# Optimization experiments

Measured on AMD Instinct MI355X. Metric: run time of the kernel, lower is better.

## Reference

```python
import jax, jax.numpy as jnp
import numpy as np

T, N, C, D, S = 512, 32, 1296, 512, 30
NORM_SCALE = 32.0
NEGINF = -1e9


def setup_inputs() -> dict:
    key = jax.random.key(0)
    k1, k2, k3, k4, k5 = jax.random.split(key, 5)
    feats = jax.random.normal(k1, (T * N, D), dtype=jnp.float32)
    classifier_weight = jax.random.normal(k2, (D, C), dtype=jnp.float32)
    labeling = jax.random.randint(k3, (N, S), 1, C)  # targets cannot be blank(0)
    logit_lgts = (T - jax.random.randint(k4, (N,), 0, 32)).astype(jnp.int32)
    labeling_lgts = (S - jax.random.randint(k5, (N,), 0, 5)).astype(jnp.int32)
    return dict(feats=feats, classifier_weight=classifier_weight,
                labeling=labeling, logit_lgts=logit_lgts, labeling_lgts=labeling_lgts)


def _ctc_loss(log_probs, labels, in_lens, lab_lens):
    # log_probs: (T, N, C); labels: (N, S); blank = 0; reduction = 'sum'
    Tt, Nn, Cc = log_probs.shape
    Ss = labels.shape[1]
    L = 2 * Ss + 1
    # extended labeling: blank, l1, blank, l2, ..., blank  -> (N, L)
    ext = jnp.zeros((Nn, L), dtype=labels.dtype).at[:, 1::2].set(labels)
    # gather per-state log-probs: (T, N, L)
    lp_ext = jnp.take_along_axis(log_probs, jnp.broadcast_to(ext[None], (Tt, Nn, L)), axis=2)
    # skip transition s-2 -> s allowed iff s > 1 and ext[s] != ext[s-2]
    skip_ok = jnp.concatenate(
        [jnp.zeros((Nn, 2), dtype=bool), ext[:, 2:] != ext[:, :-2]], axis=1)
    alpha0 = (jnp.full((Nn, L), NEGINF, dtype=log_probs.dtype)
              .at[:, 0].set(lp_ext[0, :, 0])
              .at[:, 1].set(lp_ext[0, :, 1]))

    def step(alpha, inp):
        lp_t, t = inp  # lp_t: (N, L)
        a1 = alpha
        a2 = jnp.pad(alpha[:, :-1], ((0, 0), (1, 0)), constant_values=NEGINF)
        a3 = jnp.where(skip_ok,
                       jnp.pad(alpha[:, :-2], ((0, 0), (2, 0)), constant_values=NEGINF),
                       NEGINF)
        new = jax.nn.logsumexp(jnp.stack([a1, a2, a3], axis=0), axis=0) + lp_t
        # freeze alpha once t reaches a sample's input length
        alpha = jnp.where((t < in_lens)[:, None], new, alpha)
        return alpha, None

    alpha, _ = jax.lax.scan(step, alpha0, (lp_ext[1:], jnp.arange(1, Tt)))
    Ln = 2 * lab_lens + 1  # (N,)
    last = jnp.take_along_axis(alpha, (Ln - 1)[:, None], axis=1)[:, 0]
    last2 = jnp.take_along_axis(alpha, (Ln - 2)[:, None], axis=1)[:, 0]
    nll = -jnp.logaddexp(last, last2)
    return jnp.sum(nll)


def reference(feats, classifier_weight, labeling, logit_lgts, labeling_lgts):
    # RadialCTC: cosine logits with norm_scale, then CTC on log-softmax.
    w_n = classifier_weight / jnp.linalg.norm(classifier_weight, axis=0, keepdims=True)  # (D, C)
    f_n = feats / jnp.linalg.norm(feats, axis=1, keepdims=True)  # (T*N, D)
    logits = NORM_SCALE * (f_n @ w_n)  # (T*N, C)
    log_probs = jax.nn.log_softmax(logits.reshape(T, N, C), axis=-1)
    return _ctc_loss(log_probs, labeling, logit_lgts, labeling_lgts)
```

## Files before the change

kernel.cpp:

```cpp
#include <hip/hip_runtime.h>
#include <stdint.h>
#include <stddef.h>


typedef _Float16 f16;
typedef _Float16 f16x8 __attribute__((ext_vector_type(8)));
typedef float f32x4 __attribute__((ext_vector_type(4)));
typedef __attribute__((address_space(1))) void* as1_void_ptr;
typedef __attribute__((address_space(3))) void* as3_void_ptr;

#define TT 512
#define NN 32
#define CC 1296
#define DD 512
#define SS 30
#define CP 1408
#define LL 61
#define NORM_SCALE 32.0f
#define LOG2E 1.4426950408889634f
#define LN2   0.6931471805599453f

#define PREP_WBLK (CP / 16)
#define PREP_ZBLK 17
#define PREP_FBLK (TT * NN / 4)

#define GEMM_BLK ((TT * NN / 128) * (CP / 128))
#define GATH_BLK (NN * (TT / 64))

__device__ __forceinline__ float fexp2(float x) { return __builtin_amdgcn_exp2f(x); }
__device__ __forceinline__ float flog2(float x) { return __builtin_amdgcn_logf(x); }

__device__ __forceinline__ double dpp_sr1_zero64(double x) {
    long long b = __double_as_longlong(x);
    int lo = (int)(b & 0xFFFFFFFFLL);
    int hi = (int)(b >> 32);
    int lo2 = __builtin_amdgcn_update_dpp(0, lo, 0x138, 0xF, 0xF, false);
    int hi2 = __builtin_amdgcn_update_dpp(0, hi, 0x138, 0xF, 0xF, false);
    return __longlong_as_double(((long long)hi2 << 32) |
                                (unsigned long long)(unsigned int)lo2);
}
template <int CTRL>
__device__ __forceinline__ int dpp_imax_level(int m) {
    int t = __builtin_amdgcn_update_dpp(0, m, CTRL, 0xF, 0xF, false);
    return m > t ? m : t;
}

__global__ __launch_bounds__(256) void prep_kernel(const float* __restrict__ W,
                                                   const float* __restrict__ feats,
                                                   f16* __restrict__ wt,
                                                   f16* __restrict__ fn,
                                                   float* __restrict__ sumexp,
                                                   unsigned* __restrict__ ctr) {
    int bx = blockIdx.x, tid = threadIdx.x;
    if (bx < PREP_WBLK) {
        __shared__ float red[256];
        __shared__ float rqs[16];
        int c0 = bx * 16;
        int cl = tid & 15, dg = tid >> 4;
        int c = c0 + cl;
        float ss = 0.f;
        if (c < CC) {
            for (int d = dg; d < DD; d += 16) {
                float v = W[(size_t)d * CC + c];
                ss += v * v;
            }
        }
        red[tid] = ss;
        __syncthreads();
        if (tid < 16) {
            float s2 = 0.f;
            #pragma unroll
            for (int k = 0; k < 16; ++k) s2 += red[tid + 16 * k];
            rqs[tid] = rsqrtf(s2);
        }
        __syncthreads();
        int c_loc = tid >> 4, dl = tid & 15;
        int cc = c0 + c_loc;
        float rq = rqs[c_loc];
        #pragma unroll 4
        for (int it = 0; it < 32; ++it) {
            int d = dl + it * 16;
            float v = (cc < CC) ? W[(size_t)d * CC + cc] * rq : 0.f;
            wt[(size_t)cc * DD + d] = (f16)v;
        }
    } else if (bx < PREP_WBLK + PREP_ZBLK) {
        int zb = bx - PREP_WBLK;
        if (zb < 16) {
            float4 z = {0.f, 0.f, 0.f, 0.f};
            ((float4*)sumexp)[zb * 256 + tid] = z;
        } else if (tid == 0) {
            *ctr = 0u;
        }
    } else {
        int fb = bx - PREP_WBLK - PREP_ZBLK;
        int wv = (fb * 256 + tid) >> 6;
        int lane = tid & 63;
        const float4* src = (const float4*)(feats + (size_t)wv * DD) + lane * 2;
        float4 a = src[0], b = src[1];
        float ss = a.x*a.x + a.y*a.y + a.z*a.z + a.w*a.w
                 + b.x*b.x + b.y*b.y + b.z*b.z + b.w*b.w;
        #pragma unroll
        for (int off = 32; off; off >>= 1) ss += __shfl_xor(ss, off);
        float r = rsqrtf(ss);
        f16x8 o;
        o[0]=(f16)(a.x*r); o[1]=(f16)(a.y*r); o[2]=(f16)(a.z*r); o[3]=(f16)(a.w*r);
        o[4]=(f16)(b.x*r); o[5]=(f16)(b.y*r); o[6]=(f16)(b.z*r); o[7]=(f16)(b.w*r);
        *(f16x8*)(fn + (size_t)wv * DD + lane * 8) = o;
    }
}

__global__ __launch_bounds__(256) void gg_kernel(const f16* __restrict__ A,
                                                 const f16* __restrict__ B,
                                                 const int* __restrict__ labels,
                                                 float* __restrict__ sumexp,
                                                 float* __restrict__ lp_lab) {
    __shared__ __align__(16) f16 sm[8192];
    int bx = blockIdx.x;
    int tid = threadIdx.x;
    int w = tid >> 6, lane = tid & 63;
    int lm = lane & 15, hi = lane >> 4;
    int sw = (lm >> 1) & 3;

    if (bx < GEMM_BLK) {
        int bm = bx & 127, bn = bx >> 7;
        int wm = w >> 1, wn = w & 1;
        f32x4 acc[4][4];
        f32x4 zero = {0.f, 0.f, 0.f, 0.f};
        #pragma unroll
        for (int i = 0; i < 4; ++i)
            #pragma unroll
            for (int j = 0; j < 4; ++j) acc[i][j] = zero;

        for (int kb = 0; kb < 16; ++kb) {
            #pragma unroll
            for (int p = 0; p < 2; ++p) {
                int s = p * 256 + tid;
                int row = s >> 2;
                int ch = (s & 3) ^ ((row >> 1) & 3);
                const f16* ga = A + (size_t)(bm * 128 + row) * DD + kb * 32 + ch * 8;
                const f16* gb = B + (size_t)(bn * 128 + row) * DD + kb * 32 + ch * 8;
                __builtin_amdgcn_global_load_lds((as1_void_ptr)ga,
                    (as3_void_ptr)&sm[(p * 256 + w * 64) * 8], 16, 0, 0);
                __builtin_amdgcn_global_load_lds((as1_void_ptr)gb,
                    (as3_void_ptr)&sm[4096 + (p * 256 + w * 64) * 8], 16, 0, 0);
            }
            __syncthreads();
            f16x8 af[4], bf[4];
            #pragma unroll
            for (int i = 0; i < 4; ++i)
                af[i] = *(const f16x8*)&sm[(wm * 64 + i * 16 + lm) * 32 + (hi ^ sw) * 8];
            #pragma unroll
            for (int j = 0; j < 4; ++j)
                bf[j] = *(const f16x8*)&sm[4096 + (wn * 64 + j * 16 + lm) * 32 + (hi ^ sw) * 8];
            #pragma unroll
            for (int i = 0; i < 4; ++i)
                #pragma unroll
                for (int j = 0; j < 4; ++j)
                    acc[i][j] = __builtin_amdgcn_mfma_f32_16x16x32_f16(af[i], bf[j], acc[i][j], 0, 0, 0);
            __syncthreads();
        }
        #pragma unroll
        for (int i = 0; i < 4; ++i) {
            float rs[4] = {0.f, 0.f, 0.f, 0.f};
            #pragma unroll
            for (int j = 0; j < 4; ++j) {
                int c = bn * 128 + wn * 64 + j * 16 + lm;
                bool ok = (c < CC);
                #pragma unroll
                for (int r = 0; r < 4; ++r)
                    rs[r] += ok ? fexp2(acc[i][j][r] * (NORM_SCALE * LOG2E)) : 0.f;
            }
            #pragma unroll
            for (int off = 1; off < 16; off <<= 1) {
                #pragma unroll
                for (int r = 0; r < 4; ++r) rs[r] += __shfl_xor(rs[r], off);
            }
            if (lm == 0) {
                int rowb = bm * 128 + wm * 64 + i * 16 + hi * 4;
                #pragma unroll
                for (int r = 0; r < 4; ++r) atomicAdd(&sumexp[rowb + r], rs[r]);
            }
        }
    } else {
        int gbx = bx - GEMM_BLK;
        int n = gbx & 31, t0 = (gbx >> 5) * 64;
        int arow = tid >> 2;
        int ach = (tid & 3) ^ ((arow >> 1) & 3);
        const f16* gaB = A + (size_t)((t0 + arow) * NN + n) * DD + ach * 8;
        int brow = tid >> 2;
        int bch = (tid & 3) ^ ((brow >> 1) & 3);
        int cls = (brow == 0 || brow > SS) ? 0 : labels[n * SS + brow - 1];
        const f16* gbB = B + (size_t)cls * DD + bch * 8;

        f32x4 acc0 = {0.f, 0.f, 0.f, 0.f};
        f32x4 acc1 = {0.f, 0.f, 0.f, 0.f};
        for (int kb = 0; kb < 16; ++kb) {
            __builtin_amdgcn_global_load_lds((as1_void_ptr)(gaB + kb * 32),
                (as3_void_ptr)&sm[tid * 8], 16, 0, 0);
            if (tid < 128)
                __builtin_amdgcn_global_load_lds((as1_void_ptr)(gbB + kb * 32),
                    (as3_void_ptr)&sm[2048 + tid * 8], 16, 0, 0);
            __syncthreads();
            f16x8 af  = *(const f16x8*)&sm[(w * 16 + lm) * 32 + (hi ^ sw) * 8];
            f16x8 bf0 = *(const f16x8*)&sm[2048 + lm * 32 + (hi ^ sw) * 8];
            f16x8 bf1 = *(const f16x8*)&sm[2048 + (16 + lm) * 32 + (hi ^ sw) * 8];
            acc0 = __builtin_amdgcn_mfma_f32_16x16x32_f16(af, bf0, acc0, 0, 0, 0);
            acc1 = __builtin_amdgcn_mfma_f32_16x16x32_f16(af, bf1, acc1, 0, 0, 0);
            __syncthreads();
        }
        #pragma unroll
        for (int jn = 0; jn < 2; ++jn) {
            int j = jn * 16 + lm;
            if (j >= 31) continue;
            float* dst = lp_lab + ((size_t)n * 31 + j) * TT + t0;
            f32x4 av = jn ? acc1 : acc0;
            #pragma unroll
            for (int r = 0; r < 4; ++r) {
                int tl = w * 16 + hi * 4 + r;
                dst[tl] = av[r] * (NORM_SCALE * LOG2E);
            }
        }
    }
}

__global__ void ctc_kernel(const float* __restrict__ lp_lab, const int* __restrict__ labels,
                           const int* __restrict__ in_lens, const int* __restrict__ lab_lens,
                           const float* __restrict__ sumexp,
                           float* __restrict__ nll, unsigned* __restrict__ ctr,
                           float* __restrict__ out) {
    int n = blockIdx.x;
    int s = threadIdx.x;
    bool valid = s < LL;
    int ext = (valid && (s & 1)) ? labels[n * SS + (s >> 1)] : 0;
    int jmap = (valid && (s & 1)) ? ((s >> 1) + 1) : 0;
    int ext2 = __shfl_up(ext, 2);
    double skipd = ((s >= 2) && valid && (ext != ext2)) ? 1.0 : 0.0;
    int Tin = in_lens[n];
    const float4* g0 = (const float4*)(lp_lab + ((size_t)n * 31 + jmap) * TT);

    float4 cur = g0[0];
    float4 nxt = g0[1];
    float4 nx2 = g0[2];
    double beta = (s <= 1) ? (double)fexp2(cur.x) : 0.0;
    int Mi = 0;

    auto stepL = [&](float lp) {
        double P = (double)fexp2(lp);
        double b1 = dpp_sr1_zero64(beta);
        double b2 = dpp_sr1_zero64(b1);
        beta = (beta + b1 + b2 * skipd) * P;
    };
    auto renorm = [&]() {
        int h = (int)(__double_as_longlong(beta) >> 32);
        h = dpp_imax_level<0x111>(h);
        h = dpp_imax_level<0x112>(h);
        h = dpp_imax_level<0x114>(h);
        h = dpp_imax_level<0x118>(h);
        int r0 = __builtin_amdgcn_readlane(h, 15);
        int r1 = __builtin_amdgcn_readlane(h, 31);
        int r2 = __builtin_amdgcn_readlane(h, 47);
        int r3 = __builtin_amdgcn_readlane(h, 63);
        int mx = max(max(r0, r1), max(r2, r3));
        int e11 = mx >> 20;
        double scale = __longlong_as_double((long long)(2046 - e11) << 52);
        beta *= scale;
        Mi += e11 - 1023;
    };

    stepL(cur.y); stepL(cur.z); stepL(cur.w);
    renorm();
    int remaining = Tin - 4;
    int g = 1;
    while (remaining >= 4) {
        cur = nxt; nxt = nx2;
        int gi = g + 2; if (gi > 127) gi = 127;
        nx2 = g0[gi];
        stepL(cur.x); stepL(cur.y); stepL(cur.z); stepL(cur.w);
        renorm();
        remaining -= 4; ++g;
    }
    cur = nxt;
    if (remaining > 0) stepL(cur.x);
    if (remaining > 1) stepL(cur.y);
    if (remaining > 2) stepL(cur.z);

    double ms = 0.0;
    for (int t = s; t < Tin; t += 64)
        ms += (double)flog2(sumexp[(size_t)t * NN + n]);
    #pragma unroll
    for (int off = 32; off; off >>= 1) ms += __shfl_xor(ms, off);

    int Ln = 2 * lab_lens[n] + 1;
    double last  = __shfl(beta, Ln - 1);
    double last2 = __shfl(beta, Ln - 2);
    double sm = last + last2;
    long long bb = __double_as_longlong(sm);
    int e = (int)(bb >> 52) - 1023;
    double mant = __longlong_as_double((bb & 0xFFFFFFFFFFFFFLL) | (1023LL << 52));
    float v = (float)(-((double)flog2((float)mant) + (double)(e + Mi) - ms) * LN2);
    if (s == 0) {
        nll[n] = v;
        __threadfence();
        unsigned old = atomicAdd(ctr, 1u);
        if (old == NN - 1) {
            __threadfence();
            float t = 0.f;
            for (int i = 0; i < NN; ++i) t += nll[i];
            out[0] = t;
        }
    }
}

extern "C" void kernel_launch(void* const* d_in, const int* in_sizes, int n_in,
                              void* d_out, int out_size, void* d_ws, size_t ws_size,
                              hipStream_t stream) {
    const float* feats        = (const float*)d_in[0];
    const float* W            = (const float*)d_in[1];
    const int*   labeling     = (const int*)d_in[2];
    const int*   logit_lgts   = (const int*)d_in[3];
    const int*   labeling_lgts= (const int*)d_in[4];
    float* out = (float*)d_out;
    char* ws = (char*)d_ws;

    size_t off = 0;
    f16*   wt     = (f16*)(ws + off);   off += (size_t)CP * DD * 2;
    f16*   fn     = (f16*)(ws + off);   off += (size_t)TT * NN * DD * 2;
    float* sumexp = (float*)(ws + off); off += (size_t)TT * NN * 4;
    float* lp_lab = (float*)(ws + off); off += (size_t)NN * 31 * TT * 4;
    float* nllb   = (float*)(ws + off); off += 64 * 4;
    unsigned* ctr = (unsigned*)(ws + off); off += 64;

    prep_kernel<<<PREP_WBLK + PREP_ZBLK + PREP_FBLK, 256, 0, stream>>>(
        W, feats, wt, fn, sumexp, ctr);
    gg_kernel<<<GEMM_BLK + GATH_BLK, 256, 0, stream>>>(fn, wt, labeling, sumexp, lp_lab);
    ctc_kernel<<<NN, 64, 0, stream>>>(lp_lab, labeling, logit_lgts, labeling_lgts,
                                      sumexp, nllb, ctr, out);

    (void)in_sizes; (void)n_in; (void)out_size; (void)ws_size;
}
```

Baseline: 160.7 us.

## Fuse CTC recursion into GEMM kernel with atomic-counter cross-block signaling

Merges the GEMM/gather kernel and the CTC kernel into one launch. The 32 CTC blocks come first in the grid and spin on a counter until the gather blocks finish, then run the alpha recursion while the GEMM blocks are still computing the softmax sums, and wait on a second counter only before the final normalisation. This overlaps the serial CTC recursion with the GEMM and removes one launch. The cost is that 32 blocks occupy CU slots while spinning, and correctness depends on those blocks being scheduled alongside the producer blocks.

New measurement: 312.2 us. 1.94x slower.

```diff
diff --git a/kernel.cpp b/kernel.cpp
--- a/kernel.cpp
+++ b/kernel.cpp
@@ -26,9 +26,21 @@
 
 #define GEMM_BLK ((TT * NN / 128) * (CP / 128))
 #define GATH_BLK (NN * (TT / 64))
+#define MEGA_CTC 32
+#define MEGA_GATH0 MEGA_CTC
+#define MEGA_GEMM0 (MEGA_CTC + GATH_BLK)
+#define MEGA_BLK  (MEGA_GEMM0 + GEMM_BLK)
 
 __device__ __forceinline__ float fexp2(float x) { return __builtin_amdgcn_exp2f(x); }
 __device__ __forceinline__ float flog2(float x) { return __builtin_amdgcn_logf(x); }
+
+__device__ __forceinline__ void wait_cnt(unsigned* p, unsigned target) {
+    while (__hip_atomic_load(p, __ATOMIC_ACQUIRE, __HIP_MEMORY_SCOPE_AGENT) < target)
+        __builtin_amdgcn_s_sleep(8);
+}
+__device__ __forceinline__ void post_cnt(unsigned* p) {
+    __hip_atomic_fetch_add(p, 1u, __ATOMIC_RELEASE, __HIP_MEMORY_SCOPE_AGENT);
+}
 
 __device__ __forceinline__ double dpp_sr1_zero64(double x) {
     long long b = __double_as_longlong(x);
@@ -50,7 +62,7 @@
                                                    f16* __restrict__ wt,
                                                    f16* __restrict__ fn,
                                                    float* __restrict__ sumexp,
-                                                   unsigned* __restrict__ ctr) {
+                                                   unsigned* __restrict__ cnt) {
     int bx = blockIdx.x, tid = threadIdx.x;
     if (bx < PREP_WBLK) {
         __shared__ float red[256];
@@ -88,8 +100,8 @@
         if (zb < 16) {
             float4 z = {0.f, 0.f, 0.f, 0.f};
             ((float4*)sumexp)[zb * 256 + tid] = z;
-        } else if (tid == 0) {
-            *ctr = 0u;
+        } else if (tid < 3) {
+            cnt[tid] = 0u;
         }
     } else {
         int fb = bx - PREP_WBLK - PREP_ZBLK;
@@ -109,11 +121,16 @@
     }
 }
 
-__global__ __launch_bounds__(256) void gg_kernel(const f16* __restrict__ A,
-                                                 const f16* __restrict__ B,
-                                                 const int* __restrict__ labels,
-                                                 float* __restrict__ sumexp,
-                                                 float* __restrict__ lp_lab) {
+__global__ __launch_bounds__(256) void mega_kernel(const f16* __restrict__ A,
+                                                   const f16* __restrict__ B,
+                                                   const int* __restrict__ labels,
+                                                   const int* __restrict__ in_lens,
+                                                   const int* __restrict__ lab_lens,
+                                                   float* __restrict__ sumexp,
+                                                   float* __restrict__ lp_lab,
+                                                   float* __restrict__ nll,
+                                                   unsigned* __restrict__ cnt,
+                                                   float* __restrict__ out) {
     __shared__ __align__(16) f16 sm[8192];
     int bx = blockIdx.x;
     int tid = threadIdx.x;
@@ -121,15 +138,16 @@
     int lm = lane & 15, hi = lane >> 4;
     int sw = (lm >> 1) & 3;
 
-    if (bx < GEMM_BLK) {
-        int bm = bx & 127, bn = bx >> 7;
+    if (bx >= MEGA_GEMM0) {
+        int j = bx - MEGA_GEMM0;
+        int bm = j & 127, bn = j >> 7;
         int wm = w >> 1, wn = w & 1;
         f32x4 acc[4][4];
         f32x4 zero = {0.f, 0.f, 0.f, 0.f};
         #pragma unroll
         for (int i = 0; i < 4; ++i)
             #pragma unroll
-            for (int j = 0; j < 4; ++j) acc[i][j] = zero;
+            for (int jj = 0; jj < 4; ++jj) acc[i][jj] = zero;
 
         for (int kb = 0; kb < 16; ++kb) {
             #pragma unroll
@@ -150,25 +168,25 @@
             for (int i = 0; i < 4; ++i)
                 af[i] = *(const f16x8*)&sm[(wm * 64 + i * 16 + lm) * 32 + (hi ^ sw) * 8];
             #pragma unroll
-            for (int j = 0; j < 4; ++j)
-                bf[j] = *(const f16x8*)&sm[4096 + (wn * 64 + j * 16 + lm) * 32 + (hi ^ sw) * 8];
+            for (int jj = 0; jj < 4; ++jj)
+                bf[jj] = *(const f16x8*)&sm[4096 + (wn * 64 + jj * 16 + lm) * 32 + (hi ^ sw) * 8];
             #pragma unroll
             for (int i = 0; i < 4; ++i)
                 #pragma unroll
-                for (int j = 0; j < 4; ++j)
-                    acc[i][j] = __builtin_amdgcn_mfma_f32_16x16x32_f16(af[i], bf[j], acc[i][j], 0, 0, 0);
+                for (int jj = 0; jj < 4; ++jj)
+                    acc[i][jj] = __builtin_amdgcn_mfma_f32_16x16x32_f16(af[i], bf[jj], acc[i][jj], 0, 0, 0);
             __syncthreads();
         }
         #pragma unroll
         for (int i = 0; i < 4; ++i) {
             float rs[4] = {0.f, 0.f, 0.f, 0.f};
             #pragma unroll
-            for (int j = 0; j < 4; ++j) {
-                int c = bn * 128 + wn * 64 + j * 16 + lm;
+            for (int jj = 0; jj < 4; ++jj) {
+                int c = bn * 128 + wn * 64 + jj * 16 + lm;
                 bool ok = (c < CC);
                 #pragma unroll
                 for (int r = 0; r < 4; ++r)
-                    rs[r] += ok ? fexp2(acc[i][j][r] * (NORM_SCALE * LOG2E)) : 0.f;
+                    rs[r] += ok ? fexp2(acc[i][jj][r] * (NORM_SCALE * LOG2E)) : 0.f;
             }
             #pragma unroll
             for (int off = 1; off < 16; off <<= 1) {
@@ -181,8 +199,11 @@
                 for (int r = 0; r < 4; ++r) atomicAdd(&sumexp[rowb + r], rs[r]);
             }
         }
-    } else {
-        int gbx = bx - GEMM_BLK;
+        __threadfence();
+        __syncthreads();
+        if (tid == 0) post_cnt(&cnt[1]);
+    } else if (bx >= MEGA_GATH0) {
+        int gbx = bx - MEGA_GATH0;
         int n = gbx & 31, t0 = (gbx >> 5) * 64;
         int arow = tid >> 2;
         int ach = (tid & 3) ^ ((arow >> 1) & 3);
@@ -210,9 +231,9 @@
         }
         #pragma unroll
         for (int jn = 0; jn < 2; ++jn) {
-            int j = jn * 16 + lm;
-            if (j >= 31) continue;
-            float* dst = lp_lab + ((size_t)n * 31 + j) * TT + t0;
+            int jc = jn * 16 + lm;
+            if (jc >= 31) continue;
+            float* dst = lp_lab + ((size_t)n * 31 + jc) * TT + t0;
             f32x4 av = jn ? acc1 : acc0;
             #pragma unroll
             for (int r = 0; r < 4; ++r) {
@@ -220,93 +241,94 @@
                 dst[tl] = av[r] * (NORM_SCALE * LOG2E);
             }
         }
-    }
-}
-
-__global__ void ctc_kernel(const float* __restrict__ lp_lab, const int* __restrict__ labels,
-                           const int* __restrict__ in_lens, const int* __restrict__ lab_lens,
-                           const float* __restrict__ sumexp,
-                           float* __restrict__ nll, unsigned* __restrict__ ctr,
-                           float* __restrict__ out) {
-    int n = blockIdx.x;
-    int s = threadIdx.x;
-    bool valid = s < LL;
-    int ext = (valid && (s & 1)) ? labels[n * SS + (s >> 1)] : 0;
-    int jmap = (valid && (s & 1)) ? ((s >> 1) + 1) : 0;
-    int ext2 = __shfl_up(ext, 2);
-    double skipd = ((s >= 2) && valid && (ext != ext2)) ? 1.0 : 0.0;
-    int Tin = in_lens[n];
-    const float4* g0 = (const float4*)(lp_lab + ((size_t)n * 31 + jmap) * TT);
-
-    float4 cur = g0[0];
-    float4 nxt = g0[1];
-    float4 nx2 = g0[2];
-    double beta = (s <= 1) ? (double)fexp2(cur.x) : 0.0;
-    int Mi = 0;
-
-    auto stepL = [&](float lp) {
-        double P = (double)fexp2(lp);
-        double b1 = dpp_sr1_zero64(beta);
-        double b2 = dpp_sr1_zero64(b1);
-        beta = (beta + b1 + b2 * skipd) * P;
-    };
-    auto renorm = [&]() {
-        int h = (int)(__double_as_longlong(beta) >> 32);
-        h = dpp_imax_level<0x111>(h);
-        h = dpp_imax_level<0x112>(h);
-        h = dpp_imax_level<0x114>(h);
-        h = dpp_imax_level<0x118>(h);
-        int r0 = __builtin_amdgcn_readlane(h, 15);
-        int r1 = __builtin_amdgcn_readlane(h, 31);
-        int r2 = __builtin_amdgcn_readlane(h, 47);
-        int r3 = __builtin_amdgcn_readlane(h, 63);
-        int mx = max(max(r0, r1), max(r2, r3));
-        int e11 = mx >> 20;
-        double scale = __longlong_as_double((long long)(2046 - e11) << 52);
-        beta *= scale;
-        Mi += e11 - 1023;
-    };
-
-    stepL(cur.y); stepL(cur.z); stepL(cur.w);
-    renorm();
-    int remaining = Tin - 4;
-    int g = 1;
-    while (remaining >= 4) {
-        cur = nxt; nxt = nx2;
-        int gi = g + 2; if (gi > 127) gi = 127;
-        nx2 = g0[gi];
-        stepL(cur.x); stepL(cur.y); stepL(cur.z); stepL(cur.w);
+        __threadfence();
+        __syncthreads();
+        if (tid == 0) post_cnt(&cnt[0]);
+    } else if (tid < 64) {
+        int n = bx;
+        int s = tid;
+        wait_cnt(&cnt[0], GATH_BLK);
+
+        bool valid = s < LL;
+        int ext = (valid && (s & 1)) ? labels[n * SS + (s >> 1)] : 0;
+        int jmap = (valid && (s & 1)) ? ((s >> 1) + 1) : 0;
+        int ext2 = __shfl_up(ext, 2);
+        double skipd = ((s >= 2) && valid && (ext != ext2)) ? 1.0 : 0.0;
+        int Tin = in_lens[n];
+        const float4* g0 = (const float4*)(lp_lab + ((size_t)n * 31 + jmap) * TT);
+
+        float4 cur = g0[0];
+        float4 nxt = g0[1];
+        float4 nx2 = g0[2];
+        double beta = (s <= 1) ? (double)fexp2(cur.x) : 0.0;
+        int Mi = 0;
+
+        auto stepL = [&](float lp) {
+            double P = (double)fexp2(lp);
+            double b1 = dpp_sr1_zero64(beta);
+            double b2 = dpp_sr1_zero64(b1);
+            beta = (beta + b1 + b2 * skipd) * P;
+        };
+        auto renorm = [&]() {
+            int h = (int)(__double_as_longlong(beta) >> 32);
+            h = dpp_imax_level<0x111>(h);
+            h = dpp_imax_level<0x112>(h);
+            h = dpp_imax_level<0x114>(h);
+            h = dpp_imax_level<0x118>(h);
+            int r0 = __builtin_amdgcn_readlane(h, 15);
+            int r1 = __builtin_amdgcn_readlane(h, 31);
+            int r2 = __builtin_amdgcn_readlane(h, 47);
+            int r3 = __builtin_amdgcn_readlane(h, 63);
+            int mx = max(max(r0, r1), max(r2, r3));
+            int e11 = mx >> 20;
+            double scale = __longlong_as_double((long long)(2046 - e11) << 52);
+            beta *= scale;
+            Mi += e11 - 1023;
+        };
+
+        stepL(cur.y); stepL(cur.z); stepL(cur.w);
         renorm();
-        remaining -= 4; ++g;
-    }
-    cur = nxt;
-    if (remaining > 0) stepL(cur.x);
-    if (remaining > 1) stepL(cur.y);
-    if (remaining > 2) stepL(cur.z);
-
-    double ms = 0.0;
-    for (int t = s; t < Tin; t += 64)
-        ms += (double)flog2(sumexp[(size_t)t * NN + n]);
-    #pragma unroll
-    for (int off = 32; off; off >>= 1) ms += __shfl_xor(ms, off);
-
-    int Ln = 2 * lab_lens[n] + 1;
-    double last  = __shfl(beta, Ln - 1);
-    double last2 = __shfl(beta, Ln - 2);
-    double sm = last + last2;
-    long long bb = __double_as_longlong(sm);
-    int e = (int)(bb >> 52) - 1023;
-    double mant = __longlong_as_double((bb & 0xFFFFFFFFFFFFFLL) | (1023LL << 52));
-    float v = (float)(-((double)flog2((float)mant) + (double)(e + Mi) - ms) * LN2);
-    if (s == 0) {
-        nll[n] = v;
-        __threadfence();
-        unsigned old = atomicAdd(ctr, 1u);
-        if (old == NN - 1) {
+        int remaining = Tin - 4;
+        int g = 1;
+        while (remaining >= 4) {
+            cur = nxt; nxt = nx2;
+            int gi = g + 2; if (gi > 127) gi = 127;
+            nx2 = g0[gi];
+            stepL(cur.x); stepL(cur.y); stepL(cur.z); stepL(cur.w);
+            renorm();
+            remaining -= 4; ++g;
+        }
+        cur = nxt;
+        if (remaining > 0) stepL(cur.x);
+        if (remaining > 1) stepL(cur.y);
+        if (remaining > 2) stepL(cur.z);
+
+        wait_cnt(&cnt[1], GEMM_BLK);
+
+        double ms = 0.0;
+        for (int t = s; t < Tin; t += 64)
+            ms += (double)flog2(sumexp[(size_t)t * NN + n]);
+        #pragma unroll
+        for (int off = 32; off; off >>= 1) ms += __shfl_xor(ms, off);
+
+        int Ln = 2 * lab_lens[n] + 1;
+        double last  = __shfl(beta, Ln - 1);
+        double last2 = __shfl(beta, Ln - 2);
+        double smv = last + last2;
+        long long bb = __double_as_longlong(smv);
+        int e = (int)(bb >> 52) - 1023;
+        double mant = __longlong_as_double((bb & 0xFFFFFFFFFFFFFLL) | (1023LL << 52));
+        float v = (float)(-((double)flog2((float)mant) + (double)(e + Mi) - ms) * LN2);
+        if (s == 0) {
+            nll[n] = v;
             __threadfence();
-            float t = 0.f;
-            for (int i = 0; i < NN; ++i) t += nll[i];
-            out[0] = t;
+            post_cnt(&cnt[2]);
+            if (n == 0) {
+                wait_cnt(&cnt[2], NN);
+                float t = 0.f;
+                for (int i = 0; i < NN; ++i) t += nll[i];
+                out[0] = t;
+            }
         }
     }
 }
@@ -328,13 +350,13 @@
     float* sumexp = (float*)(ws + off); off += (size_t)TT * NN * 4;
     float* lp_lab = (float*)(ws + off); off += (size_t)NN * 31 * TT * 4;
     float* nllb   = (float*)(ws + off); off += 64 * 4;
-    unsigned* ctr = (unsigned*)(ws + off); off += 64;
+    unsigned* cnt = (unsigned*)(ws + off); off += 64;
 
     prep_kernel<<<PREP_WBLK + PREP_ZBLK + PREP_FBLK, 256, 0, stream>>>(
-        W, feats, wt, fn, sumexp, ctr);
-    gg_kernel<<<GEMM_BLK + GATH_BLK, 256, 0, stream>>>(fn, wt, labeling, sumexp, lp_lab);
-    ctc_kernel<<<NN, 64, 0, stream>>>(lp_lab, labeling, logit_lgts, labeling_lgts,
-                                      sumexp, nllb, ctr, out);
+        W, feats, wt, fn, sumexp, cnt);
+    mega_kernel<<<MEGA_BLK, 256, 0, stream>>>(fn, wt, labeling, logit_lgts,
+                                              labeling_lgts, sumexp, lp_lab,
+                                              nllb, cnt, out);
 
     (void)in_sizes; (void)n_in; (void)out_size; (void)ws_size;
 }
```
